# Performance work log

Measured on AMD Instinct MI355X. Metric: run time of the kernel, lower is better.

## Reference

```python
import jax, jax.numpy as jnp
import numpy as np

B, L, DIN, DT, NOUT = 2, 144, 1024, 150, 4


def setup_inputs() -> dict:
    key = jax.random.key(0)
    ks = jax.random.split(key, 7)
    w = lambda k, shape: (jax.random.normal(k, shape, jnp.float32) * 0.02)
    return dict(
        x=jax.random.normal(ks[0], (B, L, DIN), jnp.float32),
        W_sh=w(ks[1], (DIN, DT)), b_sh=jnp.zeros((DT,), jnp.float32),
        W_st=w(ks[2], (DIN, DT)), b_st=jnp.zeros((DT,), jnp.float32),
        W_oh=w(ks[3], (DIN, DT)), b_oh=jnp.zeros((DT,), jnp.float32),
        W_ot=w(ks[4], (DIN, DT)), b_ot=jnp.zeros((DT,), jnp.float32),
        W_tri1=w(ks[5], (NOUT, DT, DT, DT)),
        W_tri2=w(ks[6], (NOUT, DT, DT, DT)),
    )


def _triaffine(x, y, z, W):
    # supar Triaffine convention: out[b,z,x,y,o] = sum_{i,k,j} x[b,x,i] W[o,i,k,j] y[b,y,j] z[b,z,k]
    w = jnp.einsum('bzk,oikj->bzoij', z, W)      # [B,L,o,d,d]
    t = jnp.einsum('bzoij,byj->bzoiy', w, y)     # [B,L,o,d,L]
    return jnp.einsum('bzoiy,bxi->bzxyo', t, x)  # [B,L,L,L,o]


def reference(x, W_sh, b_sh, W_st, b_st, W_oh, b_oh, W_ot, b_ot, W_tri1, W_tri2):
    # MLP projections (dropout is identity at eval time)
    sh = x @ W_sh + b_sh
    st = x @ W_st + b_st
    oh = x @ W_oh + b_oh
    ot = x @ W_ot + b_ot
    n = x.shape[1]
    # torch .triu() on (..., sh, st) keeps entries with sh <= st, zeros the rest
    tri = jnp.arange(n)[:, None] <= jnp.arange(n)[None, :]
    m = tri[None, :, :, None, None]
    # shstoh = Triaffine(st, rel_oh, sh) -> [b, sh, st, oh, o]; triu over (sh, st)
    s1 = _triaffine(st, oh, sh, W_tri1)
    s1 = jnp.where(m, s1, 0.0)
    # shstot = Triaffine(rel_ot, st, sh) -> [b, sh, ot, st, o]; permutes give (b, sh, st, ot, o) with triu over (sh, st)
    s2 = _triaffine(ot, st, sh, W_tri2)
    s2 = jnp.where(m, jnp.transpose(s2, (0, 1, 3, 2, 4)), 0.0)
    return jax.nn.log_softmax(s1, axis=-1), jax.nn.log_softmax(s2, axis=-1)
```

## Files before the change

### kernel.cpp

```cpp
#include <hip/hip_runtime.h>
#include <hip/hip_bf16.h>
#include <math.h>

typedef unsigned short u16;
typedef __attribute__((ext_vector_type(8))) short bf16x8;
typedef __attribute__((ext_vector_type(8))) unsigned short us8;
typedef __attribute__((ext_vector_type(4))) float f32x4;

static __device__ __forceinline__ u16 f2bf(float f) {
  __hip_bfloat16 h = __float2bfloat16(f);
  return *reinterpret_cast<u16*>(&h);
}

__global__ __launch_bounds__(256) void conv_x(const float* __restrict__ x,
                                              u16* __restrict__ xb) {
  int idx = (blockIdx.x * 256 + threadIdx.x) * 4;
  float4 v = *(const float4*)(x + idx);
  ushort4 o;
  o.x = f2bf(v.x); o.y = f2bf(v.y); o.z = f2bf(v.z); o.w = f2bf(v.w);
  *(ushort4*)(xb + idx) = o;
}

__global__ __launch_bounds__(256) void trans_wp(
    const float* __restrict__ W0, const float* __restrict__ W1,
    const float* __restrict__ W2, const float* __restrict__ W3,
    u16* __restrict__ WT4) {
  __shared__ float lds[64 * 151];
  int kt = blockIdx.x, p = blockIdx.y;
  const float* W = (p == 0) ? W0 : (p == 1) ? W1 : (p == 2) ? W2 : W3;
  for (int t = threadIdx.x; t < 64 * 150; t += 256) {
    int k = t / 150, j = t - k * 150;
    lds[k * 151 + j] = W[(size_t)(kt * 64 + k) * 150 + j];
  }
  __syncthreads();
  u16* dst = WT4 + (size_t)p * 160 * 1024 + kt * 64;
  for (int t = threadIdx.x; t < 160 * 64; t += 256) {
    int j = t >> 6, kk = t & 63;
    float v = (j < 150) ? lds[kk * 151 + j] : 0.f;
    dst[(size_t)j * 1024 + kk] = f2bf(v);
  }
}

__global__ __launch_bounds__(256) void transw2(const float* __restrict__ Wa,
                                               const float* __restrict__ Wb,
                                               u16* __restrict__ WtT) {
  __shared__ float lds[150 * 82];
  int oi = blockIdx.x, jh = blockIdx.y, tri = blockIdx.z;
  const float* W = tri ? Wb : Wa;
  const float* src = W + (size_t)oi * 22500 + jh * 80;
  for (int t = threadIdx.x; t < 150 * 40; t += 256) {
    int k = t / 40, c = t - k * 40;
    if (jh * 80 + 2 * c < 150) {
      float2 v = *(const float2*)(src + (size_t)k * 150 + 2 * c);
      *(float2*)&lds[k * 82 + 2 * c] = v;
    }
  }
  __syncthreads();
  u16* dst = WtT + (size_t)tri * 15360000 + (size_t)oi * 25600 +
             (size_t)jh * 80 * 160;
  for (int t = threadIdx.x; t < 80 * 20; t += 256) {
    int jl = t / 20, kc = t - jl * 20;
    int j = jh * 80 + jl;
    bool jlive = (j < 150);
    us8 v;
#pragma unroll
    for (int u = 0; u < 8; ++u) {
      int k = kc * 8 + u;
      float f = (jlive && k < 150) ? lds[k * 82 + jl] : 0.f;
      v[u] = f2bf(f);
    }
    *(us8*)(dst + (size_t)jl * 160 + kc * 8) = v;
  }
}

template <int STAGE>
__global__ __launch_bounds__(192) void gemm_sw(
    const u16* __restrict__ M0, const u16* __restrict__ N0,
    u16* __restrict__ C, const float* __restrict__ bias0,
    const float* __restrict__ bias1, const float* __restrict__ bias2,
    const float* __restrict__ bias3) {
  constexpr int KS = (STAGE == 0) ? 32 : 5;
  constexpr int SR = (STAGE == 0) ? 1024 : 160;
  const u16* Mb;
  const u16* Nb;
  u16* Cb = nullptr;
  if (STAGE == 0) {
    Mb = M0 + (size_t)blockIdx.x * 80 * 1024;
    Nb = N0 + (size_t)blockIdx.y * 144 * 1024;
  } else if (STAGE == 1) {
    int nt = blockIdx.x, oip = blockIdx.y, b = blockIdx.z;
    int tri = (oip >= 600) ? 1 : 0;
    int oi = oip - tri * 600;
    int o = oi / 150, i = oi - o * 150;
    Mb = M0 + (size_t)oip * 25600 + nt * 12800;
    Nb = N0 + (size_t)b * 23040;
    Cb = C + (size_t)tri * 29491200 + (size_t)b * 14745600 +
         ((size_t)o * 160 + i) * 160 + nt * 80;
  } else {
    int nt = blockIdx.x, f2p = blockIdx.y, b = blockIdx.z;
    int tri = (f2p >= 576) ? 1 : 0;
    int f2 = f2p - tri * 576;
    int z = f2 >> 2, o = f2 & 3;
    Mb = M0 + (size_t)tri * 29491200 + (size_t)b * 14745600 +
         (size_t)z * 102400 + o * 25600 + nt * 12800;
    Nb = N0 + (size_t)(tri ? 46080 : 92160) + (size_t)b * 23040;
    Cb = C + (size_t)tri * 26542080 + (size_t)b * 13271040 +
         (size_t)z * 92160 + o * 23040 + nt * 80;
  }
  int tid = threadIdx.x;
  int lane = tid & 63, wave = tid >> 6;
  int l16 = lane & 15, quad = lane >> 4;
  const u16* Mp = Mb + (size_t)l16 * SR + quad * 8;
  const u16* Np = Nb + (size_t)(wave * 48 + l16) * SR + quad * 8;
  f32x4 acc[5][3];
#pragma unroll
  for (int mi = 0; mi < 5; ++mi)
#pragma unroll
    for (int ni = 0; ni < 3; ++ni) acc[mi][ni] = (f32x4){0.f, 0.f, 0.f, 0.f};

#pragma unroll
  for (int ks = 0; ks < KS; ++ks) {
    bf16x8 mf[5], nf[3];
#pragma unroll
    for (int mi = 0; mi < 5; ++mi)
      mf[mi] = *(const bf16x8*)(Mp + (size_t)mi * 16 * SR + ks * 32);
#pragma unroll
    for (int ni = 0; ni < 3; ++ni)
      nf[ni] = *(const bf16x8*)(Np + (size_t)ni * 16 * SR + ks * 32);
#pragma unroll
    for (int mi = 0; mi < 5; ++mi)
#pragma unroll
      for (int ni = 0; ni < 3; ++ni)
        acc[mi][ni] = __builtin_amdgcn_mfma_f32_16x16x32_bf16(
            mf[mi], nf[ni], acc[mi][ni], 0, 0, 0);
  }

  if (STAGE == 0) {
    int p = blockIdx.x >> 1;
    const float* bp =
        (p == 0) ? bias0 : (p == 1) ? bias1 : (p == 2) ? bias2 : bias3;
    int jb0 = (blockIdx.x & 1) * 80;
#pragma unroll
    for (int mi = 0; mi < 5; ++mi) {
      int jb = jb0 + mi * 16 + quad * 4;
#pragma unroll
      for (int ni = 0; ni < 3; ++ni) {
        int row = blockIdx.y * 144 + wave * 48 + ni * 16 + l16;
        ushort4 pk;
        float v0 = (jb + 0 < 150) ? acc[mi][ni][0] + bp[jb + 0] : 0.f;
        float v1 = (jb + 1 < 150) ? acc[mi][ni][1] + bp[jb + 1] : 0.f;
        float v2 = (jb + 2 < 150) ? acc[mi][ni][2] + bp[jb + 2] : 0.f;
        float v3 = (jb + 3 < 150) ? acc[mi][ni][3] + bp[jb + 3] : 0.f;
        pk.x = f2bf(v0); pk.y = f2bf(v1); pk.z = f2bf(v2); pk.w = f2bf(v3);
        *(ushort4*)(C + ((size_t)p * 288 + row) * 160 + jb) = pk;
      }
    }
  } else {
#pragma unroll
    for (int mi = 0; mi < 5; ++mi) {
      int mb4 = mi * 16 + quad * 4;
#pragma unroll
      for (int ni = 0; ni < 3; ++ni) {
        int outer = wave * 48 + ni * 16 + l16;
        ushort4 pk;
        pk.x = f2bf(acc[mi][ni][0]); pk.y = f2bf(acc[mi][ni][1]);
        pk.z = f2bf(acc[mi][ni][2]); pk.w = f2bf(acc[mi][ni][3]);
        size_t off = (STAGE == 1) ? ((size_t)outer * 102400 + mb4)
                                  : ((size_t)outer * 160 + mb4);
        *(ushort4*)(Cb + off) = pk;
      }
    }
  }
}

template <int VAR>
__global__ __launch_bounds__(256) void stage3_kernel(
    const u16* __restrict__ tb, const u16* __restrict__ P,
    float* __restrict__ out, int BT) {
  int bx = blockIdx.x;
  int b = bx & 1, xt = (bx >> 1) * 48;
  int yt = blockIdx.y * 48;
  int zg = blockIdx.z;
  int tid = threadIdx.x;
  const float NL4 = -1.3862943611198906f;
  size_t obase = ((size_t)(b * 144 + zg)) * 82944;
  if (zg > xt + 47) {
    float4 v = make_float4(NL4, NL4, NL4, NL4);
    for (int p = tid; p < 2304; p += 256) {
      int xl = p / 48, yl = p - xl * 48;
      *(float4*)(out + obase + ((size_t)(xt + xl) * 144 + yt + yl) * 4) = v;
    }
    return;
  }
  int lane = tid & 63, wave = tid >> 6, l16 = lane & 15, quad = lane >> 4;
  int o = l16 & 3, rq = l16 >> 2;
  int arow0 = (VAR == 0) ? yt : xt;
  int nrow0 = (VAR == 0) ? xt : yt;
  const u16* Ap = tb + (size_t)b * BT + (size_t)zg * 92160 +
                  (size_t)o * 23040 +
                  (size_t)(arow0 + wave * 12 + rq) * 160 + quad * 8;
  const u16* Bp =
      P + (size_t)b * 23040 + (size_t)(nrow0 + l16) * 160 + quad * 8;
  f32x4 acc[3][3];
#pragma unroll
  for (int mi = 0; mi < 3; ++mi)
#pragma unroll
    for (int ni = 0; ni < 3; ++ni) acc[mi][ni] = (f32x4){0.f, 0.f, 0.f, 0.f};

#pragma unroll
  for (int ks = 0; ks < 5; ++ks) {
    bf16x8 af[3], bfr[3];
#pragma unroll
    for (int mi = 0; mi < 3; ++mi)
      af[mi] = *(const bf16x8*)(Ap + (size_t)mi * 4 * 160 + ks * 32);
#pragma unroll
    for (int ni = 0; ni < 3; ++ni)
      bfr[ni] = *(const bf16x8*)(Bp + (size_t)ni * 16 * 160 + ks * 32);
#pragma unroll
    for (int mi = 0; mi < 3; ++mi)
#pragma unroll
      for (int ni = 0; ni < 3; ++ni)
        acc[mi][ni] = __builtin_amdgcn_mfma_f32_16x16x32_bf16(
            af[mi], bfr[ni], acc[mi][ni], 0, 0, 0);
  }

#pragma unroll
  for (int mi = 0; mi < 3; ++mi) {
    int arow = arow0 + wave * 12 + mi * 4 + quad;
#pragma unroll
    for (int ni = 0; ni < 3; ++ni) {
      int nrow = nrow0 + ni * 16 + l16;
      int xg = (VAR == 0) ? nrow : arow;
      int yg = (VAR == 0) ? arow : nrow;
      float4 v;
      if (zg > xg) {
        v = make_float4(NL4, NL4, NL4, NL4);
      } else {
        float c0 = acc[mi][ni][0], c1 = acc[mi][ni][1];
        float c2 = acc[mi][ni][2], c3 = acc[mi][ni][3];
        float mx = fmaxf(fmaxf(c0, c1), fmaxf(c2, c3));
        float l = mx + logf(expf(c0 - mx) + expf(c1 - mx) + expf(c2 - mx) +
                            expf(c3 - mx));
        v = make_float4(c0 - l, c1 - l, c2 - l, c3 - l);
      }
      *(float4*)(out + obase + ((size_t)xg * 144 + yg) * 4) = v;
    }
  }
}

extern "C" void kernel_launch(void* const* d_in, const int* in_sizes, int n_in,
                              void* d_out, int out_size, void* d_ws,
                              size_t ws_size, hipStream_t stream) {
  const float* x = (const float*)d_in[0];
  const float* Wsh = (const float*)d_in[1];
  const float* bsh = (const float*)d_in[2];
  const float* Wst = (const float*)d_in[3];
  const float* bst = (const float*)d_in[4];
  const float* Woh = (const float*)d_in[5];
  const float* boh = (const float*)d_in[6];
  const float* Wot = (const float*)d_in[7];
  const float* bot = (const float*)d_in[8];
  const float* Wt1 = (const float*)d_in[9];
  const float* Wt2 = (const float*)d_in[10];

  u16* ws = (u16*)d_ws;
  u16* xb = ws;
  u16* WT4 = ws + 294912;
  u16* pAll = ws + 950272;
  u16* WtT = ws + 1134592;
  u16* wbuf = ws + 31854592;
  u16* tbuf = ws + 90836992;
  (void)ws_size;

  conv_x<<<288, 256, 0, stream>>>(x, xb);
  trans_wp<<<dim3(16, 4), 256, 0, stream>>>(Wsh, Wst, Woh, Wot, WT4);
  transw2<<<dim3(600, 2, 2), 256, 0, stream>>>(Wt1, Wt2, WtT);
  gemm_sw<0><<<dim3(8, 2), 192, 0, stream>>>(WT4, xb, pAll, bsh, bst, boh,
                                             bot);
  gemm_sw<1><<<dim3(2, 1200, 2), 192, 0, stream>>>(WtT, pAll, wbuf, nullptr,
                                                   nullptr, nullptr, nullptr);
  gemm_sw<2><<<dim3(2, 1152, 2), 192, 0, stream>>>(wbuf, pAll, tbuf, nullptr,
                                                   nullptr, nullptr, nullptr);

  float* out0 = (float*)d_out;
  float* out1 = out0 + 23887872;
  stage3_kernel<0><<<dim3(6, 3, 144), 256, 0, stream>>>(
      tbuf, pAll + 46080, out0, 13271040);
  stage3_kernel<1><<<dim3(6, 3, 144), 256, 0, stream>>>(
      tbuf + 26542080, pAll + 138240, out1, 13271040);
}
```

Baseline: 631.5 us.

## Fuse second triaffine contraction with final GEMM and log-softmax via LDS

Removes the separate stage-2 GEMM and its global intermediate buffer. A new kernel computes each 48-wide slice of the t tensor per (z, batch) into shared memory, then immediately runs the final contraction plus log-softmax from LDS. It also skips MFMA work for tiles wholly masked by the triangle and writes the constant -log(4) there instead. The cost is large register use (10x3 and 12x3 accumulator tiles) and about 64KB of LDS per block, which may lower occupancy.

```diff
diff --git a/kernel.cpp b/kernel.cpp
--- a/kernel.cpp
+++ b/kernel.cpp
@@ -87,7 +87,7 @@
   if (STAGE == 0) {
     Mb = M0 + (size_t)blockIdx.x * 80 * 1024;
     Nb = N0 + (size_t)blockIdx.y * 144 * 1024;
-  } else if (STAGE == 1) {
+  } else {
     int nt = blockIdx.x, oip = blockIdx.y, b = blockIdx.z;
     int tri = (oip >= 600) ? 1 : 0;
     int oi = oip - tri * 600;
@@ -96,16 +96,6 @@
     Nb = N0 + (size_t)b * 23040;
     Cb = C + (size_t)tri * 29491200 + (size_t)b * 14745600 +
          ((size_t)o * 160 + i) * 160 + nt * 80;
-  } else {
-    int nt = blockIdx.x, f2p = blockIdx.y, b = blockIdx.z;
-    int tri = (f2p >= 576) ? 1 : 0;
-    int f2 = f2p - tri * 576;
-    int z = f2 >> 2, o = f2 & 3;
-    Mb = M0 + (size_t)tri * 29491200 + (size_t)b * 14745600 +
-         (size_t)z * 102400 + o * 25600 + nt * 12800;
-    Nb = N0 + (size_t)(tri ? 46080 : 92160) + (size_t)b * 23040;
-    Cb = C + (size_t)tri * 26542080 + (size_t)b * 13271040 +
-         (size_t)z * 92160 + o * 23040 + nt * 80;
   }
   int tid = threadIdx.x;
   int lane = tid & 63, wave = tid >> 6;
@@ -165,85 +155,141 @@
         ushort4 pk;
         pk.x = f2bf(acc[mi][ni][0]); pk.y = f2bf(acc[mi][ni][1]);
         pk.z = f2bf(acc[mi][ni][2]); pk.w = f2bf(acc[mi][ni][3]);
-        size_t off = (STAGE == 1) ? ((size_t)outer * 102400 + mb4)
-                                  : ((size_t)outer * 160 + mb4);
-        *(ushort4*)(Cb + off) = pk;
+        *(ushort4*)(Cb + (size_t)outer * 102400 + mb4) = pk;
       }
     }
   }
 }
 
 template <int VAR>
-__global__ __launch_bounds__(256) void stage3_kernel(
-    const u16* __restrict__ tb, const u16* __restrict__ P,
-    float* __restrict__ out, int BT) {
-  int bx = blockIdx.x;
-  int b = bx & 1, xt = (bx >> 1) * 48;
-  int yt = blockIdx.y * 48;
-  int zg = blockIdx.z;
-  int tid = threadIdx.x;
+__global__ __launch_bounds__(256) void fuse23(const u16* __restrict__ wb,
+                                              const u16* __restrict__ pA,
+                                              float* __restrict__ out) {
+  constexpr int TSTR = 168;
+  __shared__ __align__(16) u16 t_lds[192 * TSTR];
+  int seg = blockIdx.x, zg = blockIdx.y, b = blockIdx.z;
+  int tid = threadIdx.x, lane = tid & 63, wave = tid >> 6;
+  int l16 = lane & 15, quad = lane >> 4;
   const float NL4 = -1.3862943611198906f;
   size_t obase = ((size_t)(b * 144 + zg)) * 82944;
-  if (zg > xt + 47) {
+
+  if (VAR == 1 && seg * 48 + 47 < zg) {
     float4 v = make_float4(NL4, NL4, NL4, NL4);
-    for (int p = tid; p < 2304; p += 256) {
-      int xl = p / 48, yl = p - xl * 48;
-      *(float4*)(out + obase + ((size_t)(xt + xl) * 144 + yt + yl) * 4) = v;
+    for (int p = tid; p < 48 * 144; p += 256) {
+      int xl = p / 144, y = p - xl * 144;
+      *(float4*)(out + obase + ((size_t)(seg * 48 + xl) * 144 + y) * 4) = v;
     }
     return;
   }
-  int lane = tid & 63, wave = tid >> 6, l16 = lane & 15, quad = lane >> 4;
-  int o = l16 & 3, rq = l16 >> 2;
-  int arow0 = (VAR == 0) ? yt : xt;
-  int nrow0 = (VAR == 0) ? xt : yt;
-  const u16* Ap = tb + (size_t)b * BT + (size_t)zg * 92160 +
-                  (size_t)o * 23040 +
-                  (size_t)(arow0 + wave * 12 + rq) * 160 + quad * 8;
-  const u16* Bp =
-      P + (size_t)b * 23040 + (size_t)(nrow0 + l16) * 160 + quad * 8;
-  f32x4 acc[3][3];
-#pragma unroll
-  for (int mi = 0; mi < 3; ++mi)
-#pragma unroll
-    for (int ni = 0; ni < 3; ++ni) acc[mi][ni] = (f32x4){0.f, 0.f, 0.f, 0.f};
+
+  {
+    const u16* wsl = wb + (size_t)b * 14745600 + (size_t)zg * 102400 +
+                     (size_t)wave * 25600 + (size_t)l16 * 160 + quad * 8;
+    const u16* np = pA + (size_t)(VAR ? 1 : 2) * 46080 + (size_t)b * 23040 +
+                    (size_t)(seg * 48 + l16) * 160 + quad * 8;
+    f32x4 aa[10][3];
+#pragma unroll
+    for (int mi = 0; mi < 10; ++mi)
+#pragma unroll
+      for (int ni = 0; ni < 3; ++ni) aa[mi][ni] = (f32x4){0.f, 0.f, 0.f, 0.f};
+#pragma unroll
+    for (int ks = 0; ks < 5; ++ks) {
+      bf16x8 mf[10], nf[3];
+#pragma unroll
+      for (int mi = 0; mi < 10; ++mi)
+        mf[mi] = *(const bf16x8*)(wsl + mi * 2560 + ks * 32);
+#pragma unroll
+      for (int ni = 0; ni < 3; ++ni)
+        nf[ni] = *(const bf16x8*)(np + (size_t)ni * 16 * 160 + ks * 32);
+#pragma unroll
+      for (int mi = 0; mi < 10; ++mi)
+#pragma unroll
+        for (int ni = 0; ni < 3; ++ni)
+          aa[mi][ni] = __builtin_amdgcn_mfma_f32_16x16x32_bf16(
+              mf[mi], nf[ni], aa[mi][ni], 0, 0, 0);
+    }
+#pragma unroll
+    for (int mi = 0; mi < 10; ++mi)
+#pragma unroll
+      for (int ni = 0; ni < 3; ++ni) {
+        int row = (ni * 16 + l16) * 4 + wave;
+        int ib = mi * 16 + quad * 4;
+        ushort4 pk;
+        pk.x = f2bf(aa[mi][ni][0]); pk.y = f2bf(aa[mi][ni][1]);
+        pk.z = f2bf(aa[mi][ni][2]); pk.w = f2bf(aa[mi][ni][3]);
+        *(ushort4*)&t_lds[row * TSTR + ib] = pk;
+      }
+  }
+  __syncthreads();
+
+  const u16* pn2 = pA + (size_t)(VAR ? 3 : 1) * 46080 + (size_t)b * 23040;
+  int nt[3];
+  bool lv[3];
+  const u16* np2[3];
+#pragma unroll
+  for (int t = 0; t < 3; ++t) {
+    nt[t] = wave + t * 4;
+    lv[t] = (nt[t] < 9) && (VAR == 1 || nt[t] * 16 + 15 >= zg);
+    int ntc = (nt[t] < 9) ? nt[t] : 0;
+    np2[t] = pn2 + (size_t)(ntc * 16 + l16) * 160 + quad * 8;
+  }
+  f32x4 ac[12][3];
+#pragma unroll
+  for (int mi = 0; mi < 12; ++mi)
+#pragma unroll
+    for (int t = 0; t < 3; ++t) ac[mi][t] = (f32x4){0.f, 0.f, 0.f, 0.f};
 
 #pragma unroll
   for (int ks = 0; ks < 5; ++ks) {
-    bf16x8 af[3], bfr[3];
-#pragma unroll
-    for (int mi = 0; mi < 3; ++mi)
-      af[mi] = *(const bf16x8*)(Ap + (size_t)mi * 4 * 160 + ks * 32);
-#pragma unroll
-    for (int ni = 0; ni < 3; ++ni)
-      bfr[ni] = *(const bf16x8*)(Bp + (size_t)ni * 16 * 160 + ks * 32);
-#pragma unroll
-    for (int mi = 0; mi < 3; ++mi)
-#pragma unroll
-      for (int ni = 0; ni < 3; ++ni)
-        acc[mi][ni] = __builtin_amdgcn_mfma_f32_16x16x32_bf16(
-            af[mi], bfr[ni], acc[mi][ni], 0, 0, 0);
-  }
-
-#pragma unroll
-  for (int mi = 0; mi < 3; ++mi) {
-    int arow = arow0 + wave * 12 + mi * 4 + quad;
-#pragma unroll
-    for (int ni = 0; ni < 3; ++ni) {
-      int nrow = nrow0 + ni * 16 + l16;
-      int xg = (VAR == 0) ? nrow : arow;
-      int yg = (VAR == 0) ? arow : nrow;
-      float4 v;
-      if (zg > xg) {
-        v = make_float4(NL4, NL4, NL4, NL4);
-      } else {
-        float c0 = acc[mi][ni][0], c1 = acc[mi][ni][1];
-        float c2 = acc[mi][ni][2], c3 = acc[mi][ni][3];
-        float mx = fmaxf(fmaxf(c0, c1), fmaxf(c2, c3));
-        float l = mx + logf(expf(c0 - mx) + expf(c1 - mx) + expf(c2 - mx) +
-                            expf(c3 - mx));
-        v = make_float4(c0 - l, c1 - l, c2 - l, c3 - l);
-      }
-      *(float4*)(out + obase + ((size_t)xg * 144 + yg) * 4) = v;
+    bf16x8 nf0 = *(const bf16x8*)(np2[0] + ks * 32);
+    bf16x8 nf1 = *(const bf16x8*)(np2[1] + ks * 32);
+    bf16x8 nf2 = *(const bf16x8*)(np2[2] + ks * 32);
+#pragma unroll
+    for (int mi = 0; mi < 12; ++mi) {
+      bf16x8 af =
+          *(const bf16x8*)&t_lds[(mi * 16 + l16) * TSTR + ks * 32 + quad * 8];
+      if (lv[0])
+        ac[mi][0] =
+            __builtin_amdgcn_mfma_f32_16x16x32_bf16(af, nf0, ac[mi][0], 0, 0, 0);
+      if (lv[1])
+        ac[mi][1] =
+            __builtin_amdgcn_mfma_f32_16x16x32_bf16(af, nf1, ac[mi][1], 0, 0, 0);
+      if (lv[2])
+        ac[mi][2] =
+            __builtin_amdgcn_mfma_f32_16x16x32_bf16(af, nf2, ac[mi][2], 0, 0, 0);
+    }
+  }
+
+#pragma unroll
+  for (int t = 0; t < 3; ++t) {
+    if (nt[t] >= 9) continue;
+    int nb = nt[t] * 16 + l16;
+    if (lv[t]) {
+#pragma unroll
+      for (int mi = 0; mi < 12; ++mi) {
+        int loc = seg * 48 + mi * 4 + quad;
+        int xg = (VAR == 0) ? nb : loc;
+        int yg = (VAR == 0) ? loc : nb;
+        float4 v;
+        if (zg > xg) {
+          v = make_float4(NL4, NL4, NL4, NL4);
+        } else {
+          float c0 = ac[mi][t][0], c1 = ac[mi][t][1];
+          float c2 = ac[mi][t][2], c3 = ac[mi][t][3];
+          float mx = fmaxf(fmaxf(c0, c1), fmaxf(c2, c3));
+          float l = mx + logf(expf(c0 - mx) + expf(c1 - mx) + expf(c2 - mx) +
+                              expf(c3 - mx));
+          v = make_float4(c0 - l, c1 - l, c2 - l, c3 - l);
+        }
+        *(float4*)(out + obase + ((size_t)xg * 144 + yg) * 4) = v;
+      }
+    } else {
+      float4 v = make_float4(NL4, NL4, NL4, NL4);
+#pragma unroll
+      for (int mi = 0; mi < 12; ++mi) {
+        int y = seg * 48 + mi * 4 + quad;
+        *(float4*)(out + obase + ((size_t)nb * 144 + y) * 4) = v;
+      }
     }
   }
 }
@@ -269,7 +315,6 @@
   u16* pAll = ws + 950272;
   u16* WtT = ws + 1134592;
   u16* wbuf = ws + 31854592;
-  u16* tbuf = ws + 90836992;
   (void)ws_size;
 
   conv_x<<<288, 256, 0, stream>>>(x, xb);
@@ -279,13 +324,9 @@
                                              bot);
   gemm_sw<1><<<dim3(2, 1200, 2), 192, 0, stream>>>(WtT, pAll, wbuf, nullptr,
                                                    nullptr, nullptr, nullptr);
-  gemm_sw<2><<<dim3(2, 1152, 2), 192, 0, stream>>>(wbuf, pAll, tbuf, nullptr,
-                                                   nullptr, nullptr, nullptr);
 
   float* out0 = (float*)d_out;
   float* out1 = out0 + 23887872;
-  stage3_kernel<0><<<dim3(6, 3, 144), 256, 0, stream>>>(
-      tbuf, pAll + 46080, out0, 13271040);
-  stage3_kernel<1><<<dim3(6, 3, 144), 256, 0, stream>>>(
-      tbuf + 26542080, pAll + 138240, out1, 13271040);
-}
+  fuse23<0><<<dim3(3, 144, 2), 256, 0, stream>>>(wbuf, pAll, out0);
+  fuse23<1><<<dim3(3, 144, 2), 256, 0, stream>>>(wbuf + 29491200, pAll, out1);
+}
```

Result: faster. 610.8 us (-3.3%).
